# Performance work log

Measured on AMD Instinct MI355X. Metric: run time of the kernel, lower is better.

## Reference

```python
import jax, jax.numpy as jnp
import numpy as np

T, N, K, E = 5, 2048, 20, 512
H, AI, BL, G1, G2, U = 64, 32, 64, 64, 64, 8
SLOPE, ALPHA = 0.01, 1.0


def gru(x, Wih, Whh, bih, bhh):
    # batch_first torch nn.GRU with h0 = 0. x: [B, L, I] -> [B, L, Hd]
    Hd = Whh.shape[1]
    def step(h, xt):
        gi = xt @ Wih.T + bih
        gh = h @ Whh.T + bhh
        ir, iz, in_ = jnp.split(gi, 3, axis=-1)
        hr, hz, hn = jnp.split(gh, 3, axis=-1)
        r = jax.nn.sigmoid(ir + hr)
        z = jax.nn.sigmoid(iz + hz)
        n = jnp.tanh(in_ + r * hn)
        h_new = (1.0 - z) * n + z * h
        return h_new, h_new
    h0 = jnp.zeros((x.shape[0], Hd), x.dtype)
    _, ys = jax.lax.scan(step, h0, jnp.swapaxes(x, 0, 1))
    return jnp.swapaxes(ys, 0, 1)


def lin_attn(x, w1, b1, w2):
    # LinearAttention: softmax over dim=2 (weights_size=1), then bmm -> [B,1,H]
    inter = jnp.tanh(x @ w1.T + b1)
    w = jax.nn.softmax(inter @ w2.T, axis=2)  # [B,L,1]
    return jnp.einsum('blk,blh->bkh', w, x)


def sgat_multi(x, W, a, adj):
    # All U SGAT heads at once. Decompose a^T [Wh_i || Wh_j] = s1_i + s2_j
    # (same math as the dense NxNx2F construction, without materializing it).
    O = W.shape[-1]
    Wh = jnp.einsum('nf,ufo->uno', x, W)                 # [U,N,O]
    s1 = jnp.einsum('uno,uo->un', Wh, a[:, :O, 0])
    s2 = jnp.einsum('uno,uo->un', Wh, a[:, O:, 0])
    e = jax.nn.leaky_relu(s1[:, :, None] + s2[:, None, :], SLOPE)  # [U,N,N]
    e = jnp.where(adj[None, :, :] > 0, e, -9e15)
    att = jax.nn.softmax(e, axis=2)
    h = jnp.einsum('unm,umo->uno', att, Wh)              # [U,N,O]
    # torch.cat over heads along feature dim -> [N, U*O]
    return jnp.transpose(h, (1, 0, 2)).reshape(x.shape[0], -1)


def setup_inputs() -> dict:
    key = jax.random.key(0)
    ks = iter(jax.random.split(key, 40))
    def nrm(shape, scale=0.1):
        return jax.random.normal(next(ks), shape, dtype=jnp.float32) * scale
    d = {}
    d['p'] = nrm((N, T, 3), 1.0)
    d['m'] = nrm((T, N, K, E), 1.0)
    adj = (jax.random.uniform(next(ks), (N, N)) < 0.05).astype(jnp.float32)
    d['adj'] = jnp.maximum(adj, jnp.eye(N, dtype=jnp.float32))
    d['Wih_p'] = nrm((3 * H, 3)); d['Whh_p'] = nrm((3 * H, H))
    d['bih_p'] = nrm((3 * H,)); d['bhh_p'] = nrm((3 * H,))
    d['Wih_m'] = nrm((3 * H, E)); d['Whh_m'] = nrm((3 * H, H))
    d['bih_m'] = nrm((3 * H,)); d['bhh_m'] = nrm((3 * H,))
    d['Wih_s'] = nrm((3 * H, H)); d['Whh_s'] = nrm((3 * H, H))
    d['bih_s'] = nrm((3 * H,)); d['bhh_s'] = nrm((3 * H,))
    for pref in ('ap', 'am', 'as'):
        d[pref + '_w1'] = nrm((AI, H)); d[pref + '_b1'] = nrm((AI,))
        d[pref + '_w2'] = nrm((1, AI))
    d['blend_W'] = nrm((BL, H, H)); d['blend_b'] = nrm((BL,))
    d['g1_W'] = nrm((U, BL, G1)); d['g1_a'] = nrm((U, 2 * G1, 1))
    d['g2_W'] = nrm((U, U * G1, G2)); d['g2_a'] = nrm((U, 2 * G2, 1))
    d['fin_W'] = nrm((1, U * G2)); d['fin_b'] = nrm((1,))
    return d


def reference(p, m, adj, Wih_p, Whh_p, bih_p, bhh_p, Wih_m, Whh_m, bih_m, bhh_m,
              Wih_s, Whh_s, bih_s, bhh_s, ap_w1, ap_b1, ap_w2, am_w1, am_b1, am_w2,
              as_w1, as_b1, as_w2, blend_W, blend_b, g1_W, g1_a, g2_W, g2_a,
              fin_W, fin_b):
    h_p = gru(p, Wih_p, Whh_p, bih_p, bhh_p)                     # [N,T,H]
    q = lin_attn(h_p, ap_w1, ap_b1, ap_w2)                       # [N,1,H]
    # all T message-days through gru_m at once (equivalent to python loop)
    h_m = gru(m.reshape(T * N, K, E), Wih_m, Whh_m, bih_m, bhh_m)
    r = lin_attn(h_m, am_w1, am_b1, am_w2).reshape(T, N, H).transpose(1, 0, 2)
    h_s = gru(r, Wih_s, Whh_s, bih_s, bhh_s)                     # [N,T,H]
    c = lin_attn(h_s, as_w1, as_b1, as_w2)                       # [N,1,H]
    # Blend: bilinear + relu
    x = jax.nn.relu(jnp.einsum('nbi,oij,nbj->nbo', q, blend_W, c) + blend_b)
    x = x.reshape(N, BL)
    z = jax.nn.elu(sgat_multi(x, g1_W, g1_a, adj), ALPHA)        # [N,U*G1]
    new_z = jax.nn.sigmoid(sgat_multi(z, g2_W, g2_a, adj))       # [N,U*G2]
    return jax.nn.sigmoid(new_z @ fin_W.T + fin_b)               # [N,1]
```

## Files before the change

kernel.cpp:

```cpp
#include <hip/hip_runtime.h>
#include <math.h>

namespace {

constexpr int T = 5, N = 2048, K = 20, E = 512;
constexpr int H = 64, U = 8;
constexpr int CAP = 512;
constexpr float SLOPE = 0.01f;

typedef __attribute__((ext_vector_type(8))) short short8;
typedef __attribute__((ext_vector_type(4))) float f32x4;

__device__ inline float sigm(float x) { return 1.0f / (1.0f + expf(-x)); }

__device__ inline void bsplit(float x, short& hi, short& lo) {
  unsigned u = __float_as_uint(x);
  hi = (short)(u >> 16);
  float r = x - __uint_as_float(u & 0xFFFF0000u);
  lo = (short)(__float_as_uint(r) >> 16);
}

__device__ inline float rdlane(float v, int lane) {
  return __int_as_float(__builtin_amdgcn_readlane(__float_as_int(v), lane));
}

__global__ __launch_bounds__(256) void k_prep(
    const float* __restrict__ WihM, const float* __restrict__ WhhM,
    const float* __restrict__ WihS, const float* __restrict__ WhhS,
    const float* __restrict__ WhhP, const float* __restrict__ Wb,
    short* __restrict__ BfM, short* __restrict__ BfS,
    float* __restrict__ WhhTm, float* __restrict__ WhhTs, float* __restrict__ WhhTp,
    float* __restrict__ Wt2)
{
  const int stride = 256 * 64;
  for (int idx = threadIdx.x + blockIdx.x * 256; idx < 192 * 512; idx += stride) {
    const int o = idx >> 9, k = idx & 511;
    short hi, lo; bsplit(WihM[idx], hi, lo);
    const long base = (long)(k >> 5) * 12288 + ((o >> 4) * 2) * 512
                    + ((k >> 3) & 3) * 128 + (o & 15) * 8 + (k & 7);
    BfM[base] = hi; BfM[base + 512] = lo;
  }
  for (int idx = threadIdx.x + blockIdx.x * 256; idx < 192 * 64; idx += stride) {
    const int o = idx >> 6, k = idx & 63;
    short hi, lo; bsplit(WihS[idx], hi, lo);
    const long base = (long)(k >> 5) * 12288 + ((o >> 4) * 2) * 512
                    + ((k >> 3) & 3) * 128 + (o & 15) * 8 + (k & 7);
    BfS[base] = hi; BfS[base + 512] = lo;
  }
  for (int idx = threadIdx.x + blockIdx.x * 256; idx < 64 * 192; idx += stride) {
    const int k2 = idx / 192, row = idx % 192;
    WhhTm[idx] = WhhM[row * 64 + k2];
    WhhTs[idx] = WhhS[row * 64 + k2];
    WhhTp[idx] = WhhP[row * 64 + k2];
  }
  for (int idx = threadIdx.x + blockIdx.x * 256; idx < 64 * 64 * 64; idx += stride) {
    const int o = idx >> 12, rem = idx & 4095, i = rem >> 6, j = rem & 63;
    Wt2[((i * 16 + (j >> 2)) * 64 + o) * 4 + (j & 3)] = Wb[(o * 64 + i) * 64 + j];
  }
}

__global__ __launch_bounds__(256) void k_prep2(
    const float* __restrict__ src, short* __restrict__ dst, const int Ksz)
{
  const int nb32 = Ksz >> 5;
  const int total = 8 * Ksz * 64;
  for (int idx = threadIdx.x + blockIdx.x * 256; idx < total; idx += 256 * 128) {
    const int u = idx / (Ksz * 64), rem = idx - u * Ksz * 64;
    const int f = rem >> 6, o = rem & 63;
    short hi, lo; bsplit(src[idx], hi, lo);
    const int col = u * 64 + o;
    const int cb = col >> 7, ntc = (col >> 4) & 7, c16 = col & 15;
    const int b = f >> 5, koct = (f >> 3) & 3, j = f & 7;
    const long base = ((long)(cb * nb32 + b)) * 8192 + (ntc * 2) * 512
                    + koct * 128 + c16 * 8 + j;
    dst[base] = hi; dst[base + 512] = lo;
  }
}

__global__ __launch_bounds__(256, 2) void k_gemm(
    const float* __restrict__ A, const short* __restrict__ Bf,
    const float* __restrict__ bias, float* __restrict__ out,
    const long row0, const int nb, const int strideA)
{
  __shared__ alignas(16) short Bc[2][24 * 512];
  const int tid = threadIdx.x, w = tid >> 6, l = tid & 63;
  const int lr = l & 15, g = l >> 4;
  const long blkrow = (long)blockIdx.x * 128;

  f32x4 acc[2][12];
  #pragma unroll
  for (int mf = 0; mf < 2; ++mf)
    #pragma unroll
    for (int nt = 0; nt < 12; ++nt) acc[mf][nt] = (f32x4){0.f, 0.f, 0.f, 0.f};

  short8 ahC[2], alC[2], ahN[2], alN[2];

  auto LOADA = [&](int b, short8* ah, short8* al) {
    #pragma unroll
    for (int mf = 0; mf < 2; ++mf) {
      const long r = blkrow + w * 32 + mf * 16 + lr;
      const float* __restrict__ src = A + (row0 + r) * (long)strideA + b * 32 + g * 8;
      const float4 v0 = *reinterpret_cast<const float4*>(src);
      const float4 v1 = *reinterpret_cast<const float4*>(src + 4);
      short h0,l0,h1,l1,h2,l2,h3,l3,h4,l4,h5,l5,h6,l6,h7,l7;
      bsplit(v0.x,h0,l0); bsplit(v0.y,h1,l1); bsplit(v0.z,h2,l2); bsplit(v0.w,h3,l3);
      bsplit(v1.x,h4,l4); bsplit(v1.y,h5,l5); bsplit(v1.z,h6,l6); bsplit(v1.w,h7,l7);
      ah[mf] = (short8){h0,h1,h2,h3,h4,h5,h6,h7};
      al[mf] = (short8){l0,l1,l2,l3,l4,l5,l6,l7};
    }
  };
  auto STAGE = [&](int buf, int b) {
    const short* __restrict__ bsrc = Bf + (long)b * 12288;
    #pragma unroll
    for (int i = 0; i < 6; ++i) {
      const int c = w + i * 4;
      __builtin_amdgcn_global_load_lds(
          (const __attribute__((address_space(1))) void*)(bsrc + c * 512 + l * 8),
          (__attribute__((address_space(3))) void*)(&Bc[buf][c * 512]), 16, 0, 0);
    }
  };

  LOADA(0, ahC, alC);
  STAGE(0, 0);
  __syncthreads();

  for (int b = 0; b < nb; ++b) {
    const bool more = (b + 1 < nb);
    if (more) { STAGE((b + 1) & 1, b + 1); LOADA(b + 1, ahN, alN); }
    const short* __restrict__ bcur = &Bc[b & 1][0];
    #pragma unroll
    for (int nt = 0; nt < 12; ++nt) {
      const short8 bh = *reinterpret_cast<const short8*>(bcur + (nt * 2 + 0) * 512 + l * 8);
      const short8 bl = *reinterpret_cast<const short8*>(bcur + (nt * 2 + 1) * 512 + l * 8);
      #pragma unroll
      for (int mf = 0; mf < 2; ++mf) {
        acc[mf][nt] = __builtin_amdgcn_mfma_f32_16x16x32_bf16(ahC[mf], bh, acc[mf][nt], 0, 0, 0);
        acc[mf][nt] = __builtin_amdgcn_mfma_f32_16x16x32_bf16(alC[mf], bh, acc[mf][nt], 0, 0, 0);
        acc[mf][nt] = __builtin_amdgcn_mfma_f32_16x16x32_bf16(ahC[mf], bl, acc[mf][nt], 0, 0, 0);
      }
    }
    __syncthreads();
    if (more) {
      #pragma unroll
      for (int mf = 0; mf < 2; ++mf) { ahC[mf] = ahN[mf]; alC[mf] = alN[mf]; }
    }
  }

  #pragma unroll
  for (int mf = 0; mf < 2; ++mf) {
    const long rbase = blkrow + w * 32 + mf * 16 + g * 4;
    #pragma unroll
    for (int nt = 0; nt < 12; ++nt) {
      const int col = nt * 16 + lr;
      const float bb = bias[col];
      #pragma unroll
      for (int i = 0; i < 4; ++i)
        out[(rbase + i) * 192 + col] = acc[mf][nt][i] + bb;
    }
  }
}

__global__ __launch_bounds__(256, 2) void k_gemmW(
    const float* __restrict__ A, const short* __restrict__ Bf2,
    float* __restrict__ Wh, const int nb, const int strideA)
{
  __shared__ alignas(16) short Bc[2][16 * 512];
  const int tid = threadIdx.x, w = tid >> 6, l = tid & 63;
  const int lr = l & 15, g = l >> 4;
  const long blkrow = (long)blockIdx.x * 128;
  const int cb = blockIdx.y;

  f32x4 acc[2][8];
  #pragma unroll
  for (int mf = 0; mf < 2; ++mf)
    #pragma unroll
    for (int nt = 0; nt < 8; ++nt) acc[mf][nt] = (f32x4){0.f, 0.f, 0.f, 0.f};

  short8 ahC[2], alC[2], ahN[2], alN[2];

  auto LOADA = [&](int b, short8* ah, short8* al) {
    #pragma unroll
    for (int mf = 0; mf < 2; ++mf) {
      const long r = blkrow + w * 32 + mf * 16 + lr;
      const float* __restrict__ src = A + r * (long)strideA + b * 32 + g * 8;
      const float4 v0 = *reinterpret_cast<const float4*>(src);
      const float4 v1 = *reinterpret_cast<const float4*>(src + 4);
      short h0,l0,h1,l1,h2,l2,h3,l3,h4,l4,h5,l5,h6,l6,h7,l7;
      bsplit(v0.x,h0,l0); bsplit(v0.y,h1,l1); bsplit(v0.z,h2,l2); bsplit(v0.w,h3,l3);
      bsplit(v1.x,h4,l4); bsplit(v1.y,h5,l5); bsplit(v1.z,h6,l6); bsplit(v1.w,h7,l7);
      ah[mf] = (short8){h0,h1,h2,h3,h4,h5,h6,h7};
      al[mf] = (short8){l0,l1,l2,l3,l4,l5,l6,l7};
    }
  };
  auto STAGE = [&](int buf, int b) {
    const short* __restrict__ bsrc = Bf2 + ((long)cb * nb + b) * 8192;
    #pragma unroll
    for (int i = 0; i < 4; ++i) {
      const int c = w + i * 4;
      __builtin_amdgcn_global_load_lds(
          (const __attribute__((address_space(1))) void*)(bsrc + c * 512 + l * 8),
          (__attribute__((address_space(3))) void*)(&Bc[buf][c * 512]), 16, 0, 0);
    }
  };

  LOADA(0, ahC, alC);
  STAGE(0, 0);
  __syncthreads();

  for (int b = 0; b < nb; ++b) {
    const bool more = (b + 1 < nb);
    if (more) { STAGE((b + 1) & 1, b + 1); LOADA(b + 1, ahN, alN); }
    const short* __restrict__ bcur = &Bc[b & 1][0];
    #pragma unroll
    for (int nt = 0; nt < 8; ++nt) {
      const short8 bh = *reinterpret_cast<const short8*>(bcur + (nt * 2 + 0) * 512 + l * 8);
      const short8 bl = *reinterpret_cast<const short8*>(bcur + (nt * 2 + 1) * 512 + l * 8);
      #pragma unroll
      for (int mf = 0; mf < 2; ++mf) {
        acc[mf][nt] = __builtin_amdgcn_mfma_f32_16x16x32_bf16(ahC[mf], bh, acc[mf][nt], 0, 0, 0);
        acc[mf][nt] = __builtin_amdgcn_mfma_f32_16x16x32_bf16(alC[mf], bh, acc[mf][nt], 0, 0, 0);
        acc[mf][nt] = __builtin_amdgcn_mfma_f32_16x16x32_bf16(ahC[mf], bl, acc[mf][nt], 0, 0, 0);
      }
    }
    __syncthreads();
    if (more) {
      #pragma unroll
      for (int mf = 0; mf < 2; ++mf) { ahC[mf] = ahN[mf]; alC[mf] = alN[mf]; }
    }
  }

  #pragma unroll
  for (int mf = 0; mf < 2; ++mf) {
    const long rbase = blkrow + w * 32 + mf * 16 + g * 4;
    #pragma unroll
    for (int nt = 0; nt < 8; ++nt) {
      const int col = cb * 128 + nt * 16 + lr;
      const int u = col >> 6, o = col & 63;
      #pragma unroll
      for (int i = 0; i < 4; ++i)
        Wh[((long)u * N + (rbase + i)) * 64 + o] = acc[mf][nt][i];
    }
  }
}

__global__ __launch_bounds__(256, 2) void k_recur(
    const float* __restrict__ gi, const float* __restrict__ WhhT,
    const float* __restrict__ bhh, float* __restrict__ rout, const int seq0)
{
  const int tid = threadIdx.x, w = tid >> 6, l = tid & 63;
  const int lseq = blockIdx.x * 4 + w;
  float wr[64], wz[64], wn[64];
  #pragma unroll
  for (int k2 = 0; k2 < 64; ++k2) {
    wr[k2] = WhhT[k2 * 192 + l];
    wz[k2] = WhhT[k2 * 192 + 64 + l];
    wn[k2] = WhhT[k2 * 192 + 128 + l];
  }
  const float bR = bhh[l], bZ = bhh[64 + l], bN = bhh[128 + l];
  const float* __restrict__ grow = gi + (long)lseq * K * 192;
  float h = 0.f, rsum = 0.f;
  float gR = grow[l], gZ = grow[64 + l], gN = grow[128 + l];
  for (int k = 0; k < K; ++k) {
    float nR = 0.f, nZ = 0.f, nN = 0.f;
    if (k + 1 < K) {
      const int off = (k + 1) * 192;
      nR = grow[off + l]; nZ = grow[off + 64 + l]; nN = grow[off + 128 + l];
    }
    float aR = bR, aZ = bZ, aN = bN;
    #pragma unroll
    for (int k2 = 0; k2 < 64; ++k2) {
      const float hk = rdlane(h, k2);
      aR += wr[k2] * hk; aZ += wz[k2] * hk; aN += wn[k2] * hk;
    }
    const float r = sigm(gR + aR);
    const float z = sigm(gZ + aZ);
    const float nn = tanhf(gN + r * aN);
    h = (1.f - z) * nn + z * h;
    rsum += h;
    gR = nR; gZ = nZ; gN = nN;
  }
  const int gseq = seq0 + lseq;
  const int tt = gseq / N, n = gseq % N;
  rout[(n * T + tt) * H + l] = rsum;
}

__global__ __launch_bounds__(256, 2) void k_recur_p(
    const float* __restrict__ p, const float* __restrict__ Wih,
    const float* __restrict__ WhhT, const float* __restrict__ bih,
    const float* __restrict__ bhh, float* __restrict__ q)
{
  const int tid = threadIdx.x, w = tid >> 6, l = tid & 63;
  const int n = blockIdx.x * 4 + w;
  float wr[64], wz[64], wn[64];
  #pragma unroll
  for (int k2 = 0; k2 < 64; ++k2) {
    wr[k2] = WhhT[k2 * 192 + l];
    wz[k2] = WhhT[k2 * 192 + 64 + l];
    wn[k2] = WhhT[k2 * 192 + 128 + l];
  }
  float iR[3], iZ[3], iN[3];
  #pragma unroll
  for (int c = 0; c < 3; ++c) {
    iR[c] = Wih[l * 3 + c];
    iZ[c] = Wih[(64 + l) * 3 + c];
    iN[c] = Wih[(128 + l) * 3 + c];
  }
  const float biR = bih[l], biZ = bih[64 + l], biN = bih[128 + l];
  const float bhR = bhh[l], bhZ = bhh[64 + l], bhN = bhh[128 + l];
  float h = 0.f, qs = 0.f;
  for (int t = 0; t < T; ++t) {
    const float x0 = p[n * 15 + t * 3], x1 = p[n * 15 + t * 3 + 1], x2 = p[n * 15 + t * 3 + 2];
    const float gR = biR + iR[0] * x0 + iR[1] * x1 + iR[2] * x2;
    const float gZ = biZ + iZ[0] * x0 + iZ[1] * x1 + iZ[2] * x2;
    const float gN = biN + iN[0] * x0 + iN[1] * x1 + iN[2] * x2;
    float aR = bhR, aZ = bhZ, aN = bhN;
    #pragma unroll
    for (int k2 = 0; k2 < 64; ++k2) {
      const float hk = rdlane(h, k2);
      aR += wr[k2] * hk; aZ += wz[k2] * hk; aN += wn[k2] * hk;
    }
    const float r = sigm(gR + aR), z = sigm(gZ + aZ);
    const float nn = tanhf(gN + r * aN);
    h = (1.f - z) * nn + z * h;
    qs += h;
  }
  q[n * H + l] = qs;
}

__global__ __launch_bounds__(256, 2) void k_recur_s(
    const float* __restrict__ gx, const float* __restrict__ WhhT,
    const float* __restrict__ bhh, float* __restrict__ c)
{
  const int tid = threadIdx.x, w = tid >> 6, l = tid & 63;
  const int n = blockIdx.x * 4 + w;
  float wr[64], wz[64], wn[64];
  #pragma unroll
  for (int k2 = 0; k2 < 64; ++k2) {
    wr[k2] = WhhT[k2 * 192 + l];
    wz[k2] = WhhT[k2 * 192 + 64 + l];
    wn[k2] = WhhT[k2 * 192 + 128 + l];
  }
  const float bR = bhh[l], bZ = bhh[64 + l], bN = bhh[128 + l];
  const float* __restrict__ grow = gx + (long)n * T * 192;
  float h = 0.f, cs = 0.f;
  for (int t = 0; t < T; ++t) {
    const float gR = grow[t * 192 + l], gZ = grow[t * 192 + 64 + l], gN = grow[t * 192 + 128 + l];
    float aR = bR, aZ = bZ, aN = bN;
    #pragma unroll
    for (int k2 = 0; k2 < 64; ++k2) {
      const float hk = rdlane(h, k2);
      aR += wr[k2] * hk; aZ += wz[k2] * hk; aN += wn[k2] * hk;
    }
    const float r = sigm(gR + aR), z = sigm(gZ + aZ);
    const float nn = tanhf(gN + r * aN);
    h = (1.f - z) * nn + z * h;
    cs += h;
  }
  c[n * H + l] = cs;
}

__global__ __launch_bounds__(256) void k_blend(
    const float* __restrict__ q, const float* __restrict__ c,
    const float* __restrict__ Wt2, const float* __restrict__ b,
    float* __restrict__ xout)
{
  __shared__ float qs[8][64];
  __shared__ alignas(16) float cs[8][64];
  const int tid = threadIdx.x;
  const int o = tid & 63, grp = tid >> 6;
  const int n0 = blockIdx.x * 8;
  for (int idx = tid; idx < 512; idx += 256) {
    qs[idx >> 6][idx & 63] = q[(n0 + (idx >> 6)) * 64 + (idx & 63)];
    cs[idx >> 6][idx & 63] = c[(n0 + (idx >> 6)) * 64 + (idx & 63)];
  }
  __syncthreads();
  const int na = grp * 2, nb = na + 1;
  float acca = b[o], accb = b[o];
  const float4* __restrict__ W4 = reinterpret_cast<const float4*>(Wt2);
  const float4* ca4 = reinterpret_cast<const float4*>(&cs[na][0]);
  const float4* cb4 = reinterpret_cast<const float4*>(&cs[nb][0]);
  for (int i = 0; i < 64; ++i) {
    float pa = 0.f, pb = 0.f;
    #pragma unroll
    for (int j4 = 0; j4 < 16; ++j4) {
      const float4 wv = W4[(i * 16 + j4) * 64 + o];
      const float4 va = ca4[j4], vb = cb4[j4];
      pa += wv.x * va.x + wv.y * va.y + wv.z * va.z + wv.w * va.w;
      pb += wv.x * vb.x + wv.y * vb.y + wv.z * vb.z + wv.w * vb.w;
    }
    acca += qs[na][i] * pa;
    accb += qs[nb][i] * pb;
  }
  xout[(n0 + na) * 64 + o] = fmaxf(acca, 0.f);
  xout[(n0 + nb) * 64 + o] = fmaxf(accb, 0.f);
}

__global__ __launch_bounds__(256) void k_compact(
    const float* __restrict__ adj, int* __restrict__ nbr, int* __restrict__ deg)
{
  const int w = threadIdx.x >> 6, lane = threadIdx.x & 63;
  const int i = blockIdx.x * 4 + w;
  int base = 0;
  for (int j0 = 0; j0 < N; j0 += 64) {
    const float v = adj[(long)i * N + j0 + lane];
    const unsigned long long mask = __ballot(v > 0.f);
    const int pre = __popcll(mask & ((1ull << lane) - 1ull));
    if (v > 0.f && base + pre < CAP) nbr[i * CAP + base + pre] = j0 + lane;
    base += __popcll(mask);
  }
  if (lane == 0) deg[i] = base < CAP ? base : CAP;
}

__global__ __launch_bounds__(256) void k_s12(
    const float* __restrict__ Wh, const float* __restrict__ a,
    float* __restrict__ s1, float* __restrict__ s2)
{
  const int nl = threadIdx.x >> 6, o = threadIdx.x & 63;
  const int n = blockIdx.x * 4 + nl, u = blockIdx.y;
  const float acc = Wh[((long)u * N + n) * 64 + o];
  float p1 = acc * a[u * 128 + o];
  float p2 = acc * a[u * 128 + 64 + o];
  #pragma unroll
  for (int d = 32; d > 0; d >>= 1) { p1 += __shfl_xor(p1, d, 64); p2 += __shfl_xor(p2, d, 64); }
  if (o == 0) { s1[u * N + n] = p1; s2[u * N + n] = p2; }
}

__global__ __launch_bounds__(256) void k_gat_attn(
    const float* __restrict__ Wh, const float* __restrict__ s1,
    const float* __restrict__ s2, const int* __restrict__ nbr,
    const int* __restrict__ deg, const int mode, float* __restrict__ out)
{
  __shared__ float ew[4][CAP];
  __shared__ int nb[4][CAP];
  const int w = threadIdx.x >> 6, lane = threadIdx.x & 63;
  const int row = blockIdx.x * 4 + w;
  const int u = row >> 11;
  const int i = row & (N - 1);
  const int d = deg[i];
  const float su = s1[u * N + i];
  float mx = -1e30f;
  for (int t = lane; t < d; t += 64) {
    const int j = nbr[i * CAP + t];
    float e = su + s2[u * N + j];
    e = e > 0.f ? e : SLOPE * e;
    ew[w][t] = e; nb[w][t] = j;
    mx = fmaxf(mx, e);
  }
  #pragma unroll
  for (int dd = 32; dd > 0; dd >>= 1) mx = fmaxf(mx, __shfl_xor(mx, dd, 64));
  float sm = 0.f;
  for (int t = lane; t < d; t += 64) {
    const float ex = expf(ew[w][t] - mx);
    ew[w][t] = ex;
    sm += ex;
  }
  #pragma unroll
  for (int dd = 32; dd > 0; dd >>= 1) sm += __shfl_xor(sm, dd, 64);
  __syncthreads();
  const float inv = 1.f / sm;
  float acc = 0.f;
  for (int t = 0; t < d; ++t) {
    const float att = ew[w][t];
    const int j = nb[w][t];
    acc += att * Wh[((long)u * N + j) * 64 + lane];
  }
  acc *= inv;
  float val;
  if (mode == 0) val = acc > 0.f ? acc : (expf(acc) - 1.f);
  else           val = 1.f / (1.f + expf(-acc));
  out[(long)i * (U * 64) + u * 64 + lane] = val;
}

__global__ __launch_bounds__(256) void k_final(
    const float* __restrict__ nz, const float* __restrict__ fw,
    const float* __restrict__ fb, float* __restrict__ out)
{
  const int w = threadIdx.x >> 6, lane = threadIdx.x & 63;
  const int n = blockIdx.x * 4 + w;
  float p = 0.f;
  #pragma unroll
  for (int f = lane; f < 512; f += 64) p += nz[(long)n * 512 + f] * fw[f];
  #pragma unroll
  for (int d = 32; d > 0; d >>= 1) p += __shfl_xor(p, d, 64);
  if (lane == 0) out[n] = 1.f / (1.f + expf(-(p + fb[0])));
}

}

extern "C" void kernel_launch(void* const* d_in, const int* in_sizes, int n_in,
                              void* d_out, int out_size, void* d_ws, size_t ws_size,
                              hipStream_t stream)
{
  const float* p     = (const float*)d_in[0];
  const float* m     = (const float*)d_in[1];
  const float* adj   = (const float*)d_in[2];
  const float* Wih_p = (const float*)d_in[3];
  const float* Whh_p = (const float*)d_in[4];
  const float* bih_p = (const float*)d_in[5];
  const float* bhh_p = (const float*)d_in[6];
  const float* Wih_m = (const float*)d_in[7];
  const float* Whh_m = (const float*)d_in[8];
  const float* bih_m = (const float*)d_in[9];
  const float* bhh_m = (const float*)d_in[10];
  const float* Wih_s = (const float*)d_in[11];
  const float* Whh_s = (const float*)d_in[12];
  const float* bih_s = (const float*)d_in[13];
  const float* bhh_s = (const float*)d_in[14];
  const float* blend_W = (const float*)d_in[24];
  const float* blend_b = (const float*)d_in[25];
  const float* g1W = (const float*)d_in[26];
  const float* g1a = (const float*)d_in[27];
  const float* g2W = (const float*)d_in[28];
  const float* g2a = (const float*)d_in[29];
  const float* finW = (const float*)d_in[30];
  const float* finb = (const float*)d_in[31];

  float* ws = (float*)d_ws;
  float* q    = ws;
  float* rr   = q + N * H;
  float* c    = rr + N * T * H;
  float* xb   = c + N * H;
  float* Wh1  = xb + N * H;
  float* s1a  = Wh1 + U * N * 64;
  float* s2a  = s1a + U * N;
  float* z    = s2a + U * N;
  float* Wh2  = z + (long)N * 512;
  float* s1b  = Wh2 + U * N * 64;
  float* s2b  = s1b + U * N;
  float* nz   = s2b + U * N;
  float* Wt2  = nz + (long)N * 512;
  float* gx   = Wt2 + 64 * 64 * 64;
  float* WhhTm = gx + (long)10240 * 192;
  float* WhhTs = WhhTm + 64 * 192;
  float* WhhTp = WhhTs + 64 * 192;
  int*   nbr  = (int*)(WhhTp + 64 * 192);
  int*   deg  = nbr + (long)N * CAP;
  short* BfM  = (short*)(deg + N);
  short* BfS  = BfM + 16 * 12288;
  short* Bf1  = BfS + 2 * 12288;
  short* Bf2  = Bf1 + 4 * 2 * 8192;
  float* gi   = (float*)(Bf2 + 4 * 16 * 8192);

  const long avail = (long)(ws_size / 4) - (gi - ws);
  const long total_seqs = (long)T * N;
  long chunk = (avail / ((long)K * 192) / 32) * 32;
  if (chunk > total_seqs) chunk = total_seqs;
  if (chunk < 32) chunk = 32;

  k_prep<<<64, 256, 0, stream>>>(Wih_m, Whh_m, Wih_s, Whh_s, Whh_p, blend_W,
                                 BfM, BfS, WhhTm, WhhTs, WhhTp, Wt2);
  k_prep2<<<128, 256, 0, stream>>>(g2W, Bf2, 512);
  k_prep2<<<128, 256, 0, stream>>>(g1W, Bf1, 64);
  k_recur_p<<<N / 4, 256, 0, stream>>>(p, Wih_p, WhhTp, bih_p, bhh_p, q);
  for (long s0 = 0; s0 < total_seqs; s0 += chunk) {
    const long cs = (total_seqs - s0) < chunk ? (total_seqs - s0) : chunk;
    const long rows = cs * K;
    k_gemm<<<(int)(rows / 128), 256, 0, stream>>>(m, BfM, bih_m, gi, s0 * K, 16, 512);
    k_recur<<<(int)(cs / 4), 256, 0, stream>>>(gi, WhhTm, bhh_m, rr, (int)s0);
  }
  k_gemm<<<80, 256, 0, stream>>>(rr, BfS, bih_s, gx, 0, 2, 64);
  k_recur_s<<<N / 4, 256, 0, stream>>>(gx, WhhTs, bhh_s, c);
  k_blend<<<N / 8, 256, 0, stream>>>(q, c, Wt2, blend_b, xb);
  k_compact<<<N / 4, 256, 0, stream>>>(adj, nbr, deg);
  k_gemmW<<<dim3(N / 128, 4), 256, 0, stream>>>(xb, Bf1, Wh1, 2, 64);
  k_s12<<<dim3(N / 4, U), 256, 0, stream>>>(Wh1, g1a, s1a, s2a);
  k_gat_attn<<<(U * N) / 4, 256, 0, stream>>>(Wh1, s1a, s2a, nbr, deg, 0, z);
  k_gemmW<<<dim3(N / 128, 4), 256, 0, stream>>>(z, Bf2, Wh2, 16, 512);
  k_s12<<<dim3(N / 4, U), 256, 0, stream>>>(Wh2, g2a, s1b, s2b);
  k_gat_attn<<<(U * N) / 4, 256, 0, stream>>>(Wh2, s1b, s2b, nbr, deg, 1, nz);
  k_final<<<N / 4, 256, 0, stream>>>(nz, finW, finb, (float*)d_out);
}
```

Baseline: 521.0 us.

## Fuse GAT score projections into Wh GEMM and unroll neighbor gather

The s1/s2 attention-score dot products move into the k_gemmW epilogue, reducing across the 16-lane column groups with shuffles, so the separate k_s12 launches and their re-read of Wh go away. The neighbor aggregation loop in k_gat_attn is unrolled by four with independent accumulators, which keeps more gathered loads in flight. Launch bounds on both GEMMs are raised to three blocks per SM, which tightens the register budget and risks spills with the larger accumulator arrays.

```diff
diff --git a/kernel.cpp b/kernel.cpp
--- a/kernel.cpp
+++ b/kernel.cpp
@@ -77,7 +77,7 @@
   }
 }
 
-__global__ __launch_bounds__(256, 2) void k_gemm(
+__global__ __launch_bounds__(256, 3) void k_gemm(
     const float* __restrict__ A, const short* __restrict__ Bf,
     const float* __restrict__ bias, float* __restrict__ out,
     const long row0, const int nb, const int strideA)
@@ -160,9 +160,11 @@
   }
 }
 
-__global__ __launch_bounds__(256, 2) void k_gemmW(
+__global__ __launch_bounds__(256, 3) void k_gemmW(
     const float* __restrict__ A, const short* __restrict__ Bf2,
-    float* __restrict__ Wh, const int nb, const int strideA)
+    const float* __restrict__ ga,
+    float* __restrict__ Wh, float* __restrict__ s1, float* __restrict__ s2,
+    const int nb, const int strideA)
 {
   __shared__ alignas(16) short Bc[2][16 * 512];
   const int tid = threadIdx.x, w = tid >> 6, l = tid & 63;
@@ -240,6 +242,25 @@
       for (int i = 0; i < 4; ++i)
         Wh[((long)u * N + (rbase + i)) * 64 + o] = acc[mf][nt][i];
     }
+    #pragma unroll
+    for (int i = 0; i < 4; ++i) {
+      const long r = rbase + i;
+      #pragma unroll
+      for (int uh = 0; uh < 2; ++uh) {
+        const int u = cb * 2 + uh;
+        float p1 = 0.f, p2 = 0.f;
+        #pragma unroll
+        for (int nt4 = 0; nt4 < 4; ++nt4) {
+          const float v = acc[mf][uh * 4 + nt4][i];
+          const int o = nt4 * 16 + lr;
+          p1 += v * ga[u * 128 + o];
+          p2 += v * ga[u * 128 + 64 + o];
+        }
+        #pragma unroll
+        for (int dd = 8; dd > 0; dd >>= 1) { p1 += __shfl_xor(p1, dd, 64); p2 += __shfl_xor(p2, dd, 64); }
+        if (lr == 0) { s1[u * N + r] = p1; s2[u * N + r] = p2; }
+      }
+    }
   }
 }
 
@@ -409,20 +430,6 @@
     base += __popcll(mask);
   }
   if (lane == 0) deg[i] = base < CAP ? base : CAP;
-}
-
-__global__ __launch_bounds__(256) void k_s12(
-    const float* __restrict__ Wh, const float* __restrict__ a,
-    float* __restrict__ s1, float* __restrict__ s2)
-{
-  const int nl = threadIdx.x >> 6, o = threadIdx.x & 63;
-  const int n = blockIdx.x * 4 + nl, u = blockIdx.y;
-  const float acc = Wh[((long)u * N + n) * 64 + o];
-  float p1 = acc * a[u * 128 + o];
-  float p2 = acc * a[u * 128 + 64 + o];
-  #pragma unroll
-  for (int d = 32; d > 0; d >>= 1) { p1 += __shfl_xor(p1, d, 64); p2 += __shfl_xor(p2, d, 64); }
-  if (o == 0) { s1[u * N + n] = p1; s2[u * N + n] = p2; }
 }
 
 __global__ __launch_bounds__(256) void k_gat_attn(
@@ -458,13 +465,21 @@
   for (int dd = 32; dd > 0; dd >>= 1) sm += __shfl_xor(sm, dd, 64);
   __syncthreads();
   const float inv = 1.f / sm;
-  float acc = 0.f;
-  for (int t = 0; t < d; ++t) {
-    const float att = ew[w][t];
-    const int j = nb[w][t];
-    acc += att * Wh[((long)u * N + j) * 64 + lane];
-  }
-  acc *= inv;
+  float a0 = 0.f, a1 = 0.f, a2 = 0.f, a3 = 0.f;
+  const float* __restrict__ whb = Wh + (long)u * N * 64 + lane;
+  int t = 0;
+  for (; t + 4 <= d; t += 4) {
+    const float e0 = ew[w][t],     e1 = ew[w][t + 1];
+    const float e2 = ew[w][t + 2], e3 = ew[w][t + 3];
+    const int j0 = nb[w][t],     j1 = nb[w][t + 1];
+    const int j2 = nb[w][t + 2], j3 = nb[w][t + 3];
+    a0 += e0 * whb[(long)j0 * 64];
+    a1 += e1 * whb[(long)j1 * 64];
+    a2 += e2 * whb[(long)j2 * 64];
+    a3 += e3 * whb[(long)j3 * 64];
+  }
+  for (; t < d; ++t) a0 += ew[w][t] * whb[(long)nb[w][t] * 64];
+  float acc = ((a0 + a1) + (a2 + a3)) * inv;
   float val;
   if (mode == 0) val = acc > 0.f ? acc : (expf(acc) - 1.f);
   else           val = 1.f / (1.f + expf(-acc));
@@ -562,11 +577,9 @@
   k_recur_s<<<N / 4, 256, 0, stream>>>(gx, WhhTs, bhh_s, c);
   k_blend<<<N / 8, 256, 0, stream>>>(q, c, Wt2, blend_b, xb);
   k_compact<<<N / 4, 256, 0, stream>>>(adj, nbr, deg);
-  k_gemmW<<<dim3(N / 128, 4), 256, 0, stream>>>(xb, Bf1, Wh1, 2, 64);
-  k_s12<<<dim3(N / 4, U), 256, 0, stream>>>(Wh1, g1a, s1a, s2a);
+  k_gemmW<<<dim3(N / 128, 4), 256, 0, stream>>>(xb, Bf1, g1a, Wh1, s1a, s2a, 2, 64);
   k_gat_attn<<<(U * N) / 4, 256, 0, stream>>>(Wh1, s1a, s2a, nbr, deg, 0, z);
-  k_gemmW<<<dim3(N / 128, 4), 256, 0, stream>>>(z, Bf2, Wh2, 16, 512);
-  k_s12<<<dim3(N / 4, U), 256, 0, stream>>>(Wh2, g2a, s1b, s2b);
+  k_gemmW<<<dim3(N / 128, 4), 256, 0, stream>>>(z, Bf2, g2a, Wh2, s1b, s2b, 16, 512);
   k_gat_attn<<<(U * N) / 4, 256, 0, stream>>>(Wh2, s1b, s2b, nbr, deg, 1, nz);
   k_final<<<N / 4, 256, 0, stream>>>(nz, finW, finb, (float*)d_out);
 }
```

After: 521.8 us. No clear change (+0.2%).
